# Performance work log

Hardware: AMD Instinct MI355X
Metric: run time of the kernel (lower is better)

The kernel has to match this reference:

```python
import jax, jax.numpy as jnp
import numpy as np

N_NODES = 100000
N_EDGES = 3200000


def setup_inputs() -> dict:
    key = jax.random.key(0)
    ks = jax.random.split(key, 20)
    x = jax.random.normal(ks[0], (N_NODES, 3), dtype=jnp.float32)
    edge_index = jax.random.randint(ks[1], (2, N_EDGES), 0, N_NODES, dtype=jnp.int64)

    def w(k, shape, fan_in):
        return jax.random.normal(k, shape, dtype=jnp.float32) * (1.0 / np.sqrt(fan_in))

    return {
        "x": x, "edge_index": edge_index,
        # layer 1: in=3, out=16, heads=2
        "W1": w(ks[2], (3, 32), 3), "a_src1": w(ks[3], (2, 16), 16), "a_dst1": w(ks[4], (2, 16), 16), "b1": jnp.zeros((32,), jnp.float32),
        # layer 2: in=32, out=16, heads=2
        "W2": w(ks[5], (32, 32), 32), "a_src2": w(ks[6], (2, 16), 16), "a_dst2": w(ks[7], (2, 16), 16), "b2": jnp.zeros((32,), jnp.float32),
        # layer 3: in=32, out=16, heads=1
        "W3": w(ks[8], (32, 16), 32), "a_src3": w(ks[9], (1, 16), 16), "a_dst3": w(ks[10], (1, 16), 16), "b3": jnp.zeros((16,), jnp.float32),
        # output linear 16 -> 1
        "Wout": w(ks[11], (16, 1), 16), "bout": jnp.zeros((1,), jnp.float32),
    }


def gat_layer(x, src, dst, W, a_src, a_dst, b, heads, ch, n):
    # h: [N, H, C]
    h = (x @ W).reshape(n, heads, ch)
    alpha_src = jnp.sum(h * a_src[None], axis=-1)  # [N, H]
    alpha_dst = jnp.sum(h * a_dst[None], axis=-1)  # [N, H]
    e = jax.nn.leaky_relu(alpha_src[src] + alpha_dst[dst], 0.2)  # [E, H]
    # segment softmax over incoming edges of each dst node
    m = jax.ops.segment_max(e, dst, num_segments=n)
    m = jnp.where(jnp.isfinite(m), m, 0.0)
    ex = jnp.exp(e - jax.lax.stop_gradient(m)[dst])
    s = jax.ops.segment_sum(ex, dst, num_segments=n)
    alpha = ex / (s[dst] + 1e-16)  # [E, H]
    out = jax.ops.segment_sum(h[src] * alpha[:, :, None], dst, num_segments=n)  # [N, H, C]
    return out.reshape(n, heads * ch) + b


def reference(x, edge_index, W1, a_src1, a_dst1, b1, W2, a_src2, a_dst2, b2,
              W3, a_src3, a_dst3, b3, Wout, bout):
    n = x.shape[0]
    loops = jnp.arange(n, dtype=edge_index.dtype)
    src = jnp.concatenate([edge_index[0], loops])  # PyG add_self_loops=True
    dst = jnp.concatenate([edge_index[1], loops])
    h = jax.nn.elu(gat_layer(x, src, dst, W1, a_src1, a_dst1, b1, 2, 16, n))
    h = jax.nn.elu(gat_layer(h, src, dst, W2, a_src2, a_dst2, b2, 2, 16, n))
    h = jax.nn.elu(gat_layer(h, src, dst, W3, a_src3, a_dst3, b3, 1, 16, n))
    embeddings = h
    out = jax.nn.sigmoid(h @ Wout + bout)
    return out, embeddings
```

## Files before the change

### kernel.cpp

```cpp
#include <hip/hip_runtime.h>
#include <hip/hip_fp16.h>
#include <math.h>

#define TPB 256
#define PMAX 128
#define PSH 10
#define PW  1024
#define CHUNK 2048
#define KPT 8
#define PCAP 38912
#define PCSTR 16

__device__ __forceinline__ float leaky02(float x) { return x > 0.f ? x : 0.2f * x; }
__device__ __forceinline__ float eluf(float x) { return x > 0.f ? x : (__expf(x) - 1.f); }


__global__ __launch_bounds__(256) void scatter_kernel(const int* __restrict__ src,
                                                      const int* __restrict__ dst,
                                                      int E, int n,
                                                      int* __restrict__ pcursor,
                                                      unsigned* __restrict__ pstage) {
  __shared__ int lcnt[4][PMAX];
  __shared__ int lbase[PMAX];
  int t = threadIdx.x;
  int wid = t >> 6;
  int Etot = E + n;
  int c0 = blockIdx.x * CHUNK;
  if (c0 >= Etot) return;
  int c1 = min(c0 + CHUNK, Etot);
  for (int j = t; j < 4 * PMAX; j += TPB) ((int*)lcnt)[j] = 0;

  int dd[KPT], ss[KPT];
  bool vv[KPT];
#pragma unroll
  for (int k = 0; k < KPT; ++k) {
    int idx = c0 + t + k * TPB;
    vv[k] = idx < c1;
    if (vv[k]) {
      if (idx < E) { ss[k] = src[idx]; dd[k] = dst[idx]; }
      else         { ss[k] = dd[k] = idx - E; }
    } else { ss[k] = 0; dd[k] = 0; }
  }
  __syncthreads();
#pragma unroll
  for (int k = 0; k < KPT; ++k)
    if (vv[k]) atomicAdd(&lcnt[wid][dd[k] >> PSH], 1);
  __syncthreads();
  if (t < PMAX) {
    int a0 = lcnt[0][t], a1 = lcnt[1][t], a2 = lcnt[2][t], a3 = lcnt[3][t];
    int tot = a0 + a1 + a2 + a3;
    lcnt[0][t] = 0; lcnt[1][t] = a0; lcnt[2][t] = a0 + a1; lcnt[3][t] = a0 + a1 + a2;
    lbase[t] = tot ? atomicAdd(&pcursor[t * PCSTR], tot) : 0;
  }
  __syncthreads();
#pragma unroll
  for (int k = 0; k < KPT; ++k) {
    if (vv[k]) {
      int p = dd[k] >> PSH;
      int sub = atomicAdd(&lcnt[wid][p], 1);
      pstage[(size_t)p * PCAP + lbase[p] + sub] =
          ((unsigned)ss[k] << PSH) | (unsigned)(dd[k] & (PW - 1));
    }
  }
}

__global__ __launch_bounds__(1024) void build_csr_kernel(const unsigned* __restrict__ pstage,
                                                         const int* __restrict__ pcursor,
                                                         int nvtx,
                                                         int* __restrict__ rowptr,
                                                         int* __restrict__ csr_src) {
  __shared__ int ssum[PMAX];
  __shared__ int lhist[PW];
  __shared__ int lcur[PW];
  int t = threadIdx.x;
  int lane = t & 63;
  int wid = t >> 6;
  int p = blockIdx.x;
  size_t rbase = (size_t)p * PCAP;
  if (t < PMAX) ssum[t] = pcursor[t * PCSTR];
  lhist[t] = 0;
  __syncthreads();
  for (int off = 1; off < PMAX; off <<= 1) {
    int a = 0;
    if (t < PMAX && t >= off) a = ssum[t - off];
    __syncthreads();
    if (t < PMAX) ssum[t] += a;
    __syncthreads();
  }
  int cnt = pcursor[p * PCSTR];
  int wbase = ssum[p] - cnt;
  int nodebase = p << PSH;
  for (int i = t; i < cnt; i += 4096) {
    unsigned w[4]; bool vv[4];
#pragma unroll
    for (int k = 0; k < 4; ++k) {
      int j = i + k * 1024;
      vv[k] = j < cnt;
      w[k] = vv[k] ? pstage[rbase + j] : 0u;
    }
#pragma unroll
    for (int k = 0; k < 4; ++k)
      if (vv[k]) atomicAdd(&lhist[w[k] & (PW - 1)], 1);
  }
  __syncthreads();
  int v = lhist[t];
  int x = v;
#pragma unroll
  for (int off = 1; off < 64; off <<= 1) {
    int u = __shfl_up(x, off);
    if (lane >= off) x += u;
  }
  if (lane == 63) lcur[wid] = x;
  __syncthreads();
  if (t < 16) {
    int wsum = lcur[t];
    int y = wsum;
#pragma unroll
    for (int off = 1; off < 16; off <<= 1) {
      int u = __shfl_up(y, off);
      if (t >= off) y += u;
    }
    lcur[t] = y - wsum;
  }
  __syncthreads();
  int acc = wbase + x + lcur[wid] - v;
  __syncthreads();
  lcur[t] = acc;
  int node = nodebase + t;
  if (node < nvtx) rowptr[node] = acc;
  __syncthreads();
  for (int i = t; i < cnt; i += 4096) {
    unsigned w[4]; bool vv[4];
#pragma unroll
    for (int k = 0; k < 4; ++k) {
      int j = i + k * 1024;
      vv[k] = j < cnt;
      w[k] = vv[k] ? pstage[rbase + j] : 0u;
    }
#pragma unroll
    for (int k = 0; k < 4; ++k) {
      if (vv[k]) {
        int pos = atomicAdd(&lcur[w[k] & (PW - 1)], 1);
        csr_src[pos] = (int)(w[k] >> PSH);
      }
    }
  }
  if (p == (int)gridDim.x - 1 && t == 0) rowptr[nvtx] = wbase + cnt;
}


template<int IN, int OUT, int H>
__global__ void transform_kernel(const float* __restrict__ x, const float* __restrict__ W,
                                 const float* __restrict__ a_src, const float* __restrict__ a_dst,
                                 __half* __restrict__ h, float* __restrict__ asrc,
                                 float* __restrict__ adst, int n) {
  __shared__ float sW[IN * OUT];
  __shared__ float sa[2 * OUT];
  for (int i = threadIdx.x; i < IN * OUT; i += blockDim.x) sW[i] = W[i];
  if (threadIdx.x < OUT) {
    sa[threadIdx.x] = a_src[threadIdx.x];
    sa[OUT + threadIdx.x] = a_dst[threadIdx.x];
  }
  __syncthreads();
  int i = blockIdx.x * blockDim.x + threadIdx.x;
  if (i >= n) return;
  float xv[IN];
#pragma unroll
  for (int k = 0; k < IN; k++) xv[k] = x[(size_t)i * IN + k];
  float hv[OUT];
#pragma unroll
  for (int j = 0; j < OUT; j++) {
    float acc = 0.f;
#pragma unroll
    for (int k = 0; k < IN; k++) acc += xv[k] * sW[k * OUT + j];
    hv[j] = acc;
  }
#pragma unroll
  for (int j = 0; j < OUT; j += 2)
    ((__half2*)h)[((size_t)i * OUT + j) >> 1] = __floats2half2_rn(hv[j], hv[j + 1]);
#pragma unroll
  for (int hh = 0; hh < H; hh++) {
    float as = 0.f, ad = 0.f;
#pragma unroll
    for (int c = 0; c < 16; c++) {
      as += hv[hh * 16 + c] * sa[hh * 16 + c];
      ad += hv[hh * 16 + c] * sa[OUT + hh * 16 + c];
    }
    asrc[i * H + hh] = as;
    adst[i * H + hh] = ad;
  }
}


template<int NIT>
__device__ __forceinline__ void gat12_gather(const float2* __restrict__ sp,
                                             const uint2* __restrict__ hfp,
                                             int q, int g, float4& acc) {
  float2 p[NIT];
#pragma unroll
  for (int it = 0; it < NIT; ++it) p[it] = sp[2 * (g + it * 8)];
  uint2 hv[NIT];
#pragma unroll
  for (int it = 0; it < NIT; ++it) hv[it] = hfp[__float_as_int(p[it].x) + q];
#pragma unroll
  for (int it = 0; it < NIT; ++it) {
    float2 fa = __half22float2(*(const __half2*)&hv[it].x);
    float2 fb = __half22float2(*(const __half2*)&hv[it].y);
    float w = p[it].y;
    acc.x += w * fa.x; acc.y += w * fa.y;
    acc.z += w * fb.x; acc.w += w * fb.y;
  }
}

__device__ __forceinline__ void gat12_gather_t(const float2* sp, const uint2* hfp,
                                               int q, int g, int cnt, float4& acc) {
  switch ((cnt + 7) >> 3) {
    case 1: gat12_gather<1>(sp, hfp, q, g, acc); break;
    case 2: gat12_gather<2>(sp, hfp, q, g, acc); break;
    case 3: gat12_gather<3>(sp, hfp, q, g, acc); break;
    case 4: gat12_gather<4>(sp, hfp, q, g, acc); break;
    case 5: gat12_gather<5>(sp, hfp, q, g, acc); break;
    case 6: gat12_gather<6>(sp, hfp, q, g, acc); break;
    case 7: gat12_gather<7>(sp, hfp, q, g, acc); break;
    default: gat12_gather<8>(sp, hfp, q, g, acc); break;
  }
}

__global__ __launch_bounds__(256) void node_gat12(
    const int* __restrict__ rowptr,
    const int* __restrict__ csr_src,
    const float* __restrict__ asrc,
    const float* __restrict__ adst,
    const __half* __restrict__ hfeat,
    const float* __restrict__ bias,
    float* __restrict__ outb,
    int n) {
  __shared__ float4 s_e[4][64];
  int wid = threadIdx.x >> 6;
  int lane = threadIdx.x & 63;
  int i = (blockIdx.x * blockDim.x + threadIdx.x) >> 6;
  if (i >= n) return;
  int start = rowptr[i];
  int d = rowptr[i + 1] - start;
  float ad0 = adst[i * 2 + 0];
  float ad1 = adst[i * 2 + 1];
  const uint2* hfp = (const uint2*)hfeat;
  const float2* asrc2 = (const float2*)asrc;
  int g = lane >> 3;
  int q = lane & 7;
  const float2* sp = (const float2*)(&s_e[wid][0]) + (q >> 2);
  float4 acc = make_float4(0.f, 0.f, 0.f, 0.f);
  float sl0 = 0.f, sl1 = 0.f;

  if (d <= 64) {
    int sidx8 = 0;
    float w0 = 0.f, w1 = 0.f;
    if (lane < d) {
      int sidx = csr_src[start + lane];
      sidx8 = sidx << 3;
      float2 av = asrc2[sidx];
      w0 = __expf(leaky02(av.x + ad0));
      w1 = __expf(leaky02(av.y + ad1));
    }
    sl0 = w0; sl1 = w1;
    s_e[wid][lane] = make_float4(__int_as_float(sidx8), w0, __int_as_float(sidx8), w1);
    gat12_gather_t(sp, hfp, q, g, d, acc);
  } else {
    for (int base = 0; base < d; base += 64) {
      int k = base + lane;
      int sidx8 = 0;
      float w0 = 0.f, w1 = 0.f;
      if (k < d) {
        int sidx = csr_src[start + k];
        sidx8 = sidx << 3;
        float2 av = asrc2[sidx];
        w0 = __expf(leaky02(av.x + ad0));
        w1 = __expf(leaky02(av.y + ad1));
        sl0 += w0; sl1 += w1;
      }
      s_e[wid][lane] = make_float4(__int_as_float(sidx8), w0, __int_as_float(sidx8), w1);
      int cnt = min(64, d - base);
      gat12_gather_t(sp, hfp, q, g, cnt, acc);
    }
  }

#pragma unroll
  for (int off = 32; off >= 1; off >>= 1) {
    sl0 += __shfl_xor(sl0, off);
    sl1 += __shfl_xor(sl1, off);
  }
#pragma unroll
  for (int off = 8; off <= 32; off <<= 1) {
    acc.x += __shfl_xor(acc.x, off);
    acc.y += __shfl_xor(acc.y, off);
    acc.z += __shfl_xor(acc.z, off);
    acc.w += __shfl_xor(acc.w, off);
  }
  if (lane < 8) {
    float inv = 1.f / (((lane >= 4) ? sl1 : sl0) + 1e-16f);
    float4 bv = ((const float4*)bias)[lane];
    float4 o;
    o.x = eluf(acc.x * inv + bv.x);
    o.y = eluf(acc.y * inv + bv.y);
    o.z = eluf(acc.z * inv + bv.z);
    o.w = eluf(acc.w * inv + bv.w);
    ((float4*)outb)[(size_t)i * 8 + lane] = o;
  }
}

template<int NIT>
__device__ __forceinline__ void gat3_gather(const float2* __restrict__ sp,
                                            const unsigned* __restrict__ hfp,
                                            int q, int g, float2& acc) {
  float2 p[NIT];
#pragma unroll
  for (int it = 0; it < NIT; ++it) p[it] = sp[g + it * 8];
  unsigned hv[NIT];
#pragma unroll
  for (int it = 0; it < NIT; ++it) hv[it] = hfp[__float_as_int(p[it].x) + q];
#pragma unroll
  for (int it = 0; it < NIT; ++it) {
    float2 f = __half22float2(*(const __half2*)&hv[it]);
    float w = p[it].y;
    acc.x += w * f.x; acc.y += w * f.y;
  }
}

__device__ __forceinline__ void gat3_gather_t(const float2* sp, const unsigned* hfp,
                                              int q, int g, int cnt, float2& acc) {
  switch ((cnt + 7) >> 3) {
    case 1: gat3_gather<1>(sp, hfp, q, g, acc); break;
    case 2: gat3_gather<2>(sp, hfp, q, g, acc); break;
    case 3: gat3_gather<3>(sp, hfp, q, g, acc); break;
    case 4: gat3_gather<4>(sp, hfp, q, g, acc); break;
    case 5: gat3_gather<5>(sp, hfp, q, g, acc); break;
    case 6: gat3_gather<6>(sp, hfp, q, g, acc); break;
    case 7: gat3_gather<7>(sp, hfp, q, g, acc); break;
    default: gat3_gather<8>(sp, hfp, q, g, acc); break;
  }
}

__global__ __launch_bounds__(256) void node_gat3(
    const int* __restrict__ rowptr,
    const int* __restrict__ csr_src,
    const float* __restrict__ asrc,
    const float* __restrict__ adst,
    const __half* __restrict__ hfeat,
    const float* __restrict__ b3,
    const float* __restrict__ Wout,
    const float* __restrict__ bout,
    float* __restrict__ out,
    int n) {
  __shared__ float2 s_hw[4][64];
  int wid = threadIdx.x >> 6;
  int lane = threadIdx.x & 63;
  int i = (blockIdx.x * blockDim.x + threadIdx.x) >> 6;
  if (i >= n) return;
  int start = rowptr[i];
  int d = rowptr[i + 1] - start;
  float ad0 = adst[i];
  const unsigned* hfp = (const unsigned*)hfeat;
  int g = lane >> 3;
  int q = lane & 7;
  const float2* sp = s_hw[wid];
  float2 acc = make_float2(0.f, 0.f);
  float sl = 0.f;

  if (d <= 64) {
    int sidx8 = 0;
    float w0 = 0.f;
    if (lane < d) {
      int sidx = csr_src[start + lane];
      sidx8 = sidx << 3;
      w0 = __expf(leaky02(asrc[sidx] + ad0));
    }
    sl = w0;
    s_hw[wid][lane] = make_float2(__int_as_float(sidx8), w0);
    gat3_gather_t(sp, hfp, q, g, d, acc);
  } else {
    for (int base = 0; base < d; base += 64) {
      int k = base + lane;
      int sidx8 = 0;
      float w0 = 0.f;
      if (k < d) {
        int sidx = csr_src[start + k];
        sidx8 = sidx << 3;
        w0 = __expf(leaky02(asrc[sidx] + ad0));
        sl += w0;
      }
      s_hw[wid][lane] = make_float2(__int_as_float(sidx8), w0);
      int cnt = min(64, d - base);
      gat3_gather_t(sp, hfp, q, g, cnt, acc);
    }
  }

#pragma unroll
  for (int off = 32; off >= 1; off >>= 1) sl += __shfl_xor(sl, off);
#pragma unroll
  for (int off = 8; off <= 32; off <<= 1) {
    acc.x += __shfl_xor(acc.x, off);
    acc.y += __shfl_xor(acc.y, off);
  }
  float z = 0.f;
  if (lane < 8) {
    float inv = 1.f / (sl + 1e-16f);
    float2 bv = ((const float2*)b3)[lane];
    float2 wv = ((const float2*)Wout)[lane];
    float2 o;
    o.x = eluf(acc.x * inv + bv.x);
    o.y = eluf(acc.y * inv + bv.y);
    ((float2*)(out + n))[(size_t)i * 8 + lane] = o;
    z = o.x * wv.x + o.y * wv.y;
  }
  z += __shfl_xor(z, 1);
  z += __shfl_xor(z, 2);
  z += __shfl_xor(z, 4);
  if (lane == 0) out[i] = 1.f / (1.f + __expf(-(z + bout[0])));
}


extern "C" void kernel_launch(void* const* d_in, const int* in_sizes, int n_in,
                              void* d_out, int out_size, void* d_ws, size_t ws_size,
                              hipStream_t stream) {
  const float* x    = (const float*)d_in[0];
  const int*   ei   = (const int*)d_in[1];
  const float* W1   = (const float*)d_in[2];
  const float* as1  = (const float*)d_in[3];
  const float* ad1  = (const float*)d_in[4];
  const float* b1   = (const float*)d_in[5];
  const float* W2   = (const float*)d_in[6];
  const float* as2  = (const float*)d_in[7];
  const float* ad2  = (const float*)d_in[8];
  const float* b2   = (const float*)d_in[9];
  const float* W3   = (const float*)d_in[10];
  const float* as3  = (const float*)d_in[11];
  const float* ad3  = (const float*)d_in[12];
  const float* b3   = (const float*)d_in[13];
  const float* Wout = (const float*)d_in[14];
  const float* bout = (const float*)d_in[15];
  float* out = (float*)d_out;

  const int n = in_sizes[0] / 3;
  const int E = in_sizes[1] / 2;
  const int Etot = E + n;
  const int* src = ei;
  const int* dst = ei + E;
  const int nbC = (Etot + CHUNK - 1) / CHUNK;
  const int NP = ((n - 1) >> PSH) + 1;

  float* ws = (float*)d_ws;
  float* bufH = ws;
  float* bufX = bufH + (size_t)n * 32;
  float* asrc = bufX + (size_t)n * 32;
  float* adst = asrc + (size_t)n * 2;
  int* rowptr  = (int*)(adst + (size_t)n * 2);
  int* pcursor = rowptr + n + 1;
  int* csr_src = pcursor + PMAX * PCSTR;
  unsigned* pstage = (unsigned*)ws;
  __half* hH = (__half*)bufH;

  const int nbN = (n + TPB - 1) / TPB;
  const int nbW = (n + 3) / 4;

  hipMemsetAsync(pcursor, 0, PMAX * PCSTR * sizeof(int), stream);
  scatter_kernel<<<nbC, TPB, 0, stream>>>(src, dst, E, n, pcursor, pstage);
  build_csr_kernel<<<NP, 1024, 0, stream>>>(pstage, pcursor, n, rowptr, csr_src);

  transform_kernel<3, 32, 2><<<nbN, TPB, 0, stream>>>(x, W1, as1, ad1, hH, asrc, adst, n);
  node_gat12<<<nbW, TPB, 0, stream>>>(rowptr, csr_src, asrc, adst, hH, b1, bufX, n);

  transform_kernel<32, 32, 2><<<nbN, TPB, 0, stream>>>(bufX, W2, as2, ad2, hH, asrc, adst, n);
  node_gat12<<<nbW, TPB, 0, stream>>>(rowptr, csr_src, asrc, adst, hH, b2, bufX, n);

  transform_kernel<32, 16, 1><<<nbN, TPB, 0, stream>>>(bufX, W3, as3, ad3, hH, asrc, adst, n);
  node_gat3<<<nbW, TPB, 0, stream>>>(rowptr, csr_src, asrc, adst, hH, b3, Wout, bout, out, n);
}
```

Before: 352.2 us.

## Process two nodes per wavefront using 32-lane half-waves in GAT aggregation

```diff
diff --git a/kernel.cpp b/kernel.cpp
--- a/kernel.cpp
+++ b/kernel.cpp
@@ -198,7 +198,7 @@
                                              int q, int g, float4& acc) {
   float2 p[NIT];
 #pragma unroll
-  for (int it = 0; it < NIT; ++it) p[it] = sp[2 * (g + it * 8)];
+  for (int it = 0; it < NIT; ++it) p[it] = sp[2 * (g + it * 4)];
   uint2 hv[NIT];
 #pragma unroll
   for (int it = 0; it < NIT; ++it) hv[it] = hfp[__float_as_int(p[it].x) + q];
@@ -214,7 +214,7 @@
 
 __device__ __forceinline__ void gat12_gather_t(const float2* sp, const uint2* hfp,
                                                int q, int g, int cnt, float4& acc) {
-  switch ((cnt + 7) >> 3) {
+  switch ((cnt + 3) >> 2) {
     case 1: gat12_gather<1>(sp, hfp, q, g, acc); break;
     case 2: gat12_gather<2>(sp, hfp, q, g, acc); break;
     case 3: gat12_gather<3>(sp, hfp, q, g, acc); break;
@@ -236,9 +236,11 @@
     float* __restrict__ outb,
     int n) {
   __shared__ float4 s_e[4][64];
-  int wid = threadIdx.x >> 6;
-  int lane = threadIdx.x & 63;
-  int i = (blockIdx.x * blockDim.x + threadIdx.x) >> 6;
+  int t = threadIdx.x;
+  int wid = t >> 6;
+  int sub = t & 31;
+  int half = (t >> 5) & 1;
+  int i = (blockIdx.x * TPB + t) >> 5;
   if (i >= n) return;
   int start = rowptr[i];
   int d = rowptr[i + 1] - start;
@@ -246,65 +248,48 @@
   float ad1 = adst[i * 2 + 1];
   const uint2* hfp = (const uint2*)hfeat;
   const float2* asrc2 = (const float2*)asrc;
-  int g = lane >> 3;
-  int q = lane & 7;
-  const float2* sp = (const float2*)(&s_e[wid][0]) + (q >> 2);
+  int g = sub >> 3;
+  int q = sub & 7;
+  const float2* sp = (const float2*)(&s_e[wid][half * 32]) + (q >> 2);
   float4 acc = make_float4(0.f, 0.f, 0.f, 0.f);
   float sl0 = 0.f, sl1 = 0.f;
 
-  if (d <= 64) {
+  for (int base = 0; base < d; base += 32) {
+    int k = base + sub;
     int sidx8 = 0;
     float w0 = 0.f, w1 = 0.f;
-    if (lane < d) {
-      int sidx = csr_src[start + lane];
+    if (k < d) {
+      int sidx = csr_src[start + k];
       sidx8 = sidx << 3;
       float2 av = asrc2[sidx];
       w0 = __expf(leaky02(av.x + ad0));
       w1 = __expf(leaky02(av.y + ad1));
-    }
-    sl0 = w0; sl1 = w1;
-    s_e[wid][lane] = make_float4(__int_as_float(sidx8), w0, __int_as_float(sidx8), w1);
-    gat12_gather_t(sp, hfp, q, g, d, acc);
-  } else {
-    for (int base = 0; base < d; base += 64) {
-      int k = base + lane;
-      int sidx8 = 0;
-      float w0 = 0.f, w1 = 0.f;
-      if (k < d) {
-        int sidx = csr_src[start + k];
-        sidx8 = sidx << 3;
-        float2 av = asrc2[sidx];
-        w0 = __expf(leaky02(av.x + ad0));
-        w1 = __expf(leaky02(av.y + ad1));
-        sl0 += w0; sl1 += w1;
-      }
-      s_e[wid][lane] = make_float4(__int_as_float(sidx8), w0, __int_as_float(sidx8), w1);
-      int cnt = min(64, d - base);
-      gat12_gather_t(sp, hfp, q, g, cnt, acc);
-    }
-  }
-
-#pragma unroll
-  for (int off = 32; off >= 1; off >>= 1) {
+      sl0 += w0; sl1 += w1;
+    }
+    s_e[wid][half * 32 + sub] = make_float4(__int_as_float(sidx8), w0,
+                                            __int_as_float(sidx8), w1);
+    int cnt = min(32, d - base);
+    gat12_gather_t(sp, hfp, q, g, cnt, acc);
+  }
+
+#pragma unroll
+  for (int off = 16; off >= 1; off >>= 1) {
     sl0 += __shfl_xor(sl0, off);
     sl1 += __shfl_xor(sl1, off);
   }
-#pragma unroll
-  for (int off = 8; off <= 32; off <<= 1) {
-    acc.x += __shfl_xor(acc.x, off);
-    acc.y += __shfl_xor(acc.y, off);
-    acc.z += __shfl_xor(acc.z, off);
-    acc.w += __shfl_xor(acc.w, off);
-  }
-  if (lane < 8) {
-    float inv = 1.f / (((lane >= 4) ? sl1 : sl0) + 1e-16f);
-    float4 bv = ((const float4*)bias)[lane];
+  acc.x += __shfl_xor(acc.x, 8);  acc.y += __shfl_xor(acc.y, 8);
+  acc.z += __shfl_xor(acc.z, 8);  acc.w += __shfl_xor(acc.w, 8);
+  acc.x += __shfl_xor(acc.x, 16); acc.y += __shfl_xor(acc.y, 16);
+  acc.z += __shfl_xor(acc.z, 16); acc.w += __shfl_xor(acc.w, 16);
+  if (sub < 8) {
+    float inv = 1.f / (((sub >= 4) ? sl1 : sl0) + 1e-16f);
+    float4 bv = ((const float4*)bias)[sub];
     float4 o;
     o.x = eluf(acc.x * inv + bv.x);
     o.y = eluf(acc.y * inv + bv.y);
     o.z = eluf(acc.z * inv + bv.z);
     o.w = eluf(acc.w * inv + bv.w);
-    ((float4*)outb)[(size_t)i * 8 + lane] = o;
+    ((float4*)outb)[(size_t)i * 8 + sub] = o;
   }
 }
 
@@ -314,7 +299,7 @@
                                             int q, int g, float2& acc) {
   float2 p[NIT];
 #pragma unroll
-  for (int it = 0; it < NIT; ++it) p[it] = sp[g + it * 8];
+  for (int it = 0; it < NIT; ++it) p[it] = sp[g + it * 4];
   unsigned hv[NIT];
 #pragma unroll
   for (int it = 0; it < NIT; ++it) hv[it] = hfp[__float_as_int(p[it].x) + q];
@@ -328,7 +313,7 @@
 
 __device__ __forceinline__ void gat3_gather_t(const float2* sp, const unsigned* hfp,
                                               int q, int g, int cnt, float2& acc) {
-  switch ((cnt + 7) >> 3) {
+  switch ((cnt + 3) >> 2) {
     case 1: gat3_gather<1>(sp, hfp, q, g, acc); break;
     case 2: gat3_gather<2>(sp, hfp, q, g, acc); break;
     case 3: gat3_gather<3>(sp, hfp, q, g, acc); break;
@@ -352,70 +337,56 @@
     float* __restrict__ out,
     int n) {
   __shared__ float2 s_hw[4][64];
-  int wid = threadIdx.x >> 6;
-  int lane = threadIdx.x & 63;
-  int i = (blockIdx.x * blockDim.x + threadIdx.x) >> 6;
+  int t = threadIdx.x;
+  int wid = t >> 6;
+  int sub = t & 31;
+  int half = (t >> 5) & 1;
+  int i = (blockIdx.x * TPB + t) >> 5;
   if (i >= n) return;
   int start = rowptr[i];
   int d = rowptr[i + 1] - start;
   float ad0 = adst[i];
   const unsigned* hfp = (const unsigned*)hfeat;
-  int g = lane >> 3;
-  int q = lane & 7;
-  const float2* sp = s_hw[wid];
+  int g = sub >> 3;
+  int q = sub & 7;
+  const float2* sp = &s_hw[wid][half * 32];
   float2 acc = make_float2(0.f, 0.f);
   float sl = 0.f;
 
-  if (d <= 64) {
+  for (int base = 0; base < d; base += 32) {
+    int k = base + sub;
     int sidx8 = 0;
     float w0 = 0.f;
-    if (lane < d) {
-      int sidx = csr_src[start + lane];
+    if (k < d) {
+      int sidx = csr_src[start + k];
       sidx8 = sidx << 3;
       w0 = __expf(leaky02(asrc[sidx] + ad0));
-    }
-    sl = w0;
-    s_hw[wid][lane] = make_float2(__int_as_float(sidx8), w0);
-    gat3_gather_t(sp, hfp, q, g, d, acc);
-  } else {
-    for (int base = 0; base < d; base += 64) {
-      int k = base + lane;
-      int sidx8 = 0;
-      float w0 = 0.f;
-      if (k < d) {
-        int sidx = csr_src[start + k];
-        sidx8 = sidx << 3;
-        w0 = __expf(leaky02(asrc[sidx] + ad0));
-        sl += w0;
-      }
-      s_hw[wid][lane] = make_float2(__int_as_float(sidx8), w0);
-      int cnt = min(64, d - base);
-      gat3_gather_t(sp, hfp, q, g, cnt, acc);
-    }
-  }
-
-#pragma unroll
-  for (int off = 32; off >= 1; off >>= 1) sl += __shfl_xor(sl, off);
-#pragma unroll
-  for (int off = 8; off <= 32; off <<= 1) {
-    acc.x += __shfl_xor(acc.x, off);
-    acc.y += __shfl_xor(acc.y, off);
-  }
+      sl += w0;
+    }
+    s_hw[wid][half * 32 + sub] = make_float2(__int_as_float(sidx8), w0);
+    int cnt = min(32, d - base);
+    gat3_gather_t(sp, hfp, q, g, cnt, acc);
+  }
+
+#pragma unroll
+  for (int off = 16; off >= 1; off >>= 1) sl += __shfl_xor(sl, off);
+  acc.x += __shfl_xor(acc.x, 8);  acc.y += __shfl_xor(acc.y, 8);
+  acc.x += __shfl_xor(acc.x, 16); acc.y += __shfl_xor(acc.y, 16);
   float z = 0.f;
-  if (lane < 8) {
+  if (sub < 8) {
     float inv = 1.f / (sl + 1e-16f);
-    float2 bv = ((const float2*)b3)[lane];
-    float2 wv = ((const float2*)Wout)[lane];
+    float2 bv = ((const float2*)b3)[sub];
+    float2 wv = ((const float2*)Wout)[sub];
     float2 o;
     o.x = eluf(acc.x * inv + bv.x);
     o.y = eluf(acc.y * inv + bv.y);
-    ((float2*)(out + n))[(size_t)i * 8 + lane] = o;
+    ((float2*)(out + n))[(size_t)i * 8 + sub] = o;
     z = o.x * wv.x + o.y * wv.y;
   }
   z += __shfl_xor(z, 1);
   z += __shfl_xor(z, 2);
   z += __shfl_xor(z, 4);
-  if (lane == 0) out[i] = 1.f / (1.f + __expf(-(z + bout[0])));
+  if (sub == 0) out[i] = 1.f / (1.f + __expf(-(z + bout[0])));
 }
 
 
@@ -460,7 +431,7 @@
   __half* hH = (__half*)bufH;
 
   const int nbN = (n + TPB - 1) / TPB;
-  const int nbW = (n + 3) / 4;
+  const int nbW = (n + 7) / 8;
 
   hipMemsetAsync(pcursor, 0, PMAX * PCSTR * sizeof(int), stream);
   scatter_kernel<<<nbC, TPB, 0, stream>>>(src, dst, E, n, pcursor, pstage);
```

New measurement: 346.8 us (median of 2 runs). Within noise of the previous version (-1.5%).
